# Performance work log

Measured on AMD Instinct MI355X. Metric: run time of the kernel, lower is better.

The kernel has to match this reference:

```python
import jax, jax.numpy as jnp
import numpy as np

N, E = 50000, 1600000
DIM_IN, HEADS, DIM_OUT = 256, 4, 32
NEG_SLOPE = 0.2


def setup_inputs() -> dict:
    key = jax.random.key(0)
    k1, k2, k3, k4, k5, k6 = jax.random.split(key, 6)
    x = jax.random.normal(k1, (N, DIM_IN), dtype=jnp.float32)
    edge_index = jax.random.randint(k2, (2, E), 0, N, dtype=jnp.int64)
    s = 1.0 / np.sqrt(DIM_IN)
    W = jax.random.normal(k3, (DIM_IN, HEADS * DIM_OUT), dtype=jnp.float32) * s
    att_src = jax.random.normal(k4, (HEADS, DIM_OUT), dtype=jnp.float32) * 0.1
    att_dst = jax.random.normal(k5, (HEADS, DIM_OUT), dtype=jnp.float32) * 0.1
    bias = jax.random.normal(k6, (HEADS * DIM_OUT,), dtype=jnp.float32) * 0.01
    return {"x": x, "edge_index": edge_index, "W": W,
            "att_src": att_src, "att_dst": att_dst, "bias": bias}


def reference(x, edge_index, W, att_src, att_dst, bias):
    n = x.shape[0]
    h, c = att_src.shape
    # linear projection, per-head view [N, H, C]
    xp = (x @ W).reshape(n, h, c)
    # per-node attention logits [N, H]
    a_src = jnp.einsum('nhc,hc->nh', xp, att_src)
    a_dst = jnp.einsum('nhc,hc->nh', xp, att_dst)
    # add self loops (PyG default add_self_loops=True)
    loops = jnp.arange(n, dtype=edge_index.dtype)
    src = jnp.concatenate([edge_index[0], loops])  # [E+N]
    dst = jnp.concatenate([edge_index[1], loops])
    # edge attention scores [E+N, H]
    e = jax.nn.leaky_relu(a_src[src] + a_dst[dst], negative_slope=NEG_SLOPE)
    # segment softmax over incoming edges of each dst node
    emax = jax.ops.segment_max(e, dst, num_segments=n)
    ex = jnp.exp(e - emax[dst])
    denom = jax.ops.segment_sum(ex, dst, num_segments=n)
    alpha = ex / denom[dst]  # [E+N, H]
    # weighted scatter-aggregate of src features
    msg = xp[src] * alpha[:, :, None]  # [E+N, H, C]
    out = jax.ops.segment_sum(msg, dst, num_segments=n)  # [N, H, C]
    return out.reshape(n, h * c) + bias
```

## Files before the change

### kernel.cpp

```cpp
#include <hip/hip_runtime.h>
#include <hip/hip_fp16.h>


#define DIN 256
#define HC 128
#define NH 4
#define NEG 0.2f
#define BSH 8
#define BSZ 256

typedef _Float16 half8 __attribute__((ext_vector_type(8)));
typedef _Float16 half2v __attribute__((ext_vector_type(2)));
typedef float f32x4 __attribute__((ext_vector_type(4)));

__global__ void zero_kernel(int* __restrict__ p, int n) {
    int i = blockIdx.x * blockDim.x + threadIdx.x;
    if (i < n) p[i] = 0;
}

__global__ __launch_bounds__(256) void wtrans_kernel(const float* __restrict__ W,
                                                     _Float16* __restrict__ Wt) {
    int i = blockIdx.x * 256 + threadIdx.x;
    int k = i >> 7, c = i & 127;
    Wt[c * 256 + k] = (_Float16)W[i];
}

__global__ __launch_bounds__(256) void proj_kernel(const float* __restrict__ x,
                                                   const _Float16* __restrict__ Wt,
                                                   const float* __restrict__ attS,
                                                   const float* __restrict__ attD,
                                                   __half* __restrict__ xph,
                                                   float* __restrict__ a_src,
                                                   float* __restrict__ a_dst, int n) {
    __shared__ _Float16 smem[8704];
    __shared__ float attSL[128], attDL[128];
    _Float16* xs = smem;
    _Float16* Wl = smem + 2560;
    _Float16* ep = smem;

    const int tid  = threadIdx.x;
    const int node0 = blockIdx.x * 64;
    const int wave = tid >> 6;
    const int lane = tid & 63;
    const int l15  = lane & 15;
    const int quad = lane >> 4;

    if (tid < 128) attSL[tid] = attS[tid];
    else           attDL[tid - 128] = attD[tid - 128];

    f32x4 acc[8];
#pragma unroll
    for (int ct = 0; ct < 8; ++ct) acc[ct] = (f32x4){0.f, 0.f, 0.f, 0.f};

    for (int kt = 0; kt < DIN; kt += 32) {
        __syncthreads();
#pragma unroll
        for (int r = 0; r < 4; ++r) {
            int idx = tid + r * 256;
            int row = idx >> 4;
            int kp  = idx & 15;
            int gn = node0 + row;
            float2 xv = make_float2(0.f, 0.f);
            if (gn < n) xv = *(const float2*)&x[(size_t)gn * DIN + kt + kp * 2];
            half2v p; p[0] = (_Float16)xv.x; p[1] = (_Float16)xv.y;
            *(half2v*)&xs[row * 40 + kp * 2] = p;
        }
#pragma unroll
        for (int r = 0; r < 2; ++r) {
            int id = tid + r * 256;
            int c = id >> 2;
            int q = id & 3;
            half8 wv = *(const half8*)&Wt[(size_t)c * 256 + kt + q * 8];
            *(half8*)&Wl[c * 40 + q * 8] = wv;
        }
        __syncthreads();
        half8 af = *(const half8*)&xs[(wave * 16 + l15) * 40 + quad * 8];
#pragma unroll
        for (int ct = 0; ct < 8; ++ct) {
            half8 bf = *(const half8*)&Wl[(ct * 16 + l15) * 40 + quad * 8];
            acc[ct] = __builtin_amdgcn_mfma_f32_16x16x32_f16(af, bf, acc[ct], 0, 0, 0);
        }
    }
    __syncthreads();
#pragma unroll
    for (int ct = 0; ct < 8; ++ct)
#pragma unroll
        for (int r = 0; r < 4; ++r) {
            int row = wave * 16 + quad * 4 + r;
            ep[row * 136 + ct * 16 + l15] = (_Float16)acc[ct][r];
        }
    __syncthreads();
    {
        int row = tid >> 2, ch = tid & 3;
        int node = node0 + row;
        if (node < n) {
            const uint4* s = (const uint4*)&ep[row * 136 + ch * 32];
            uint4* d = (uint4*)&xph[(size_t)node * HC + ch * 32];
            d[0] = s[0]; d[1] = s[1]; d[2] = s[2]; d[3] = s[3];
        }
    }
    {
        int nl = tid >> 2, h = tid & 3;
        int node = node0 + nl;
        if (node < n) {
            float ps = 0.f, pd = 0.f;
            const _Float16* er = &ep[nl * 136 + h * 32];
#pragma unroll
            for (int c = 0; c < 32; ++c) {
                float v = (float)er[c];
                ps += v * attSL[h * 32 + c];
                pd += v * attDL[h * 32 + c];
            }
            a_src[node * NH + h] = ps;
            a_dst[node * NH + h] = pd;
        }
    }
}

__global__ __launch_bounds__(256) void hist_kernel(const int* __restrict__ ei,
                                                   int* __restrict__ ghist, int e, int n) {
    __shared__ int h[256];
    const int tid = threadIdx.x;
    h[tid] = 0;
    __syncthreads();
    const int base = blockIdx.x * 4096;
#pragma unroll
    for (int j = 0; j < 16; ++j) {
        int i = base + j * 256 + tid;
        if (i < e) {
            int dst = ei[e + i];
            if ((unsigned)dst < (unsigned)n) atomicAdd(&h[dst >> BSH], 1);
        }
    }
    __syncthreads();
    if (h[tid]) atomicAdd(&ghist[tid], h[tid]);
}

__global__ __launch_bounds__(256) void bscan_kernel(const int* __restrict__ ghist,
                                                    int* __restrict__ gbase,
                                                    int* __restrict__ gcur, int nbuck) {
    __shared__ int buf[256];
    const int tid = threadIdx.x;
    int v = (tid < nbuck) ? ghist[tid] : 0;
    buf[tid] = v;
    __syncthreads();
    for (int s = 1; s < 256; s <<= 1) {
        int t = (tid >= s) ? buf[tid - s] : 0;
        __syncthreads();
        buf[tid] += t;
        __syncthreads();
    }
    int excl = buf[tid] - v;
    if (tid < nbuck) { gbase[tid] = excl; gcur[tid] = excl; }
    if (tid == nbuck - 1) gbase[nbuck] = buf[tid];
}

__global__ __launch_bounds__(256) void bin_kernel(const int* __restrict__ ei,
                                                  int* __restrict__ gcur,
                                                  unsigned* __restrict__ binned,
                                                  int e, int n) {
    __shared__ int h[256];
    __shared__ int rbase[256];
    const int tid = threadIdx.x;
    h[tid] = 0;
    __syncthreads();
    const int base = blockIdx.x * 4096;
    unsigned pk[16];
    int bk[16];
#pragma unroll
    for (int j = 0; j < 16; ++j) {
        int i = base + j * 256 + tid;
        bk[j] = -1;
        if (i < e) {
            int src = ei[i];
            int dst = ei[e + i];
            if ((unsigned)dst < (unsigned)n && (unsigned)src < (unsigned)n) {
                bk[j] = dst >> BSH;
                pk[j] = ((unsigned)(dst & (BSZ - 1)) << 24) | (unsigned)src;
                atomicAdd(&h[bk[j]], 1);
            }
        }
    }
    __syncthreads();
    if (h[tid]) rbase[tid] = atomicAdd(&gcur[tid], h[tid]);
    h[tid] = 0;
    __syncthreads();
#pragma unroll
    for (int j = 0; j < 16; ++j) {
        if (bk[j] >= 0) {
            int p = atomicAdd(&h[bk[j]], 1);
            binned[rbase[bk[j]] + p] = pk[j];
        }
    }
}

__global__ __launch_bounds__(256) void csr_kernel(const unsigned* __restrict__ binned,
                                                  const int* __restrict__ gbase,
                                                  int* __restrict__ off,
                                                  unsigned* __restrict__ srt,
                                                  int n, int nbuck) {
    __shared__ int cnt[256], buf[256], cur[256];
    const int tid = threadIdx.x;
    const int b = blockIdx.x;
    const int kb = gbase[b];
    const int ke = gbase[b + 1];
    cnt[tid] = 0;
    __syncthreads();
    for (int i = kb + tid; i < ke; i += 256)
        atomicAdd(&cnt[binned[i] >> 24], 1);
    __syncthreads();
    int v = cnt[tid];
    buf[tid] = v;
    __syncthreads();
    for (int s = 1; s < 256; s <<= 1) {
        int t = (tid >= s) ? buf[tid - s] : 0;
        __syncthreads();
        buf[tid] += t;
        __syncthreads();
    }
    const int excl = kb + buf[tid] - v;
    const int node = b * BSZ + tid;
    if (node < n) off[node] = excl;
    if (tid == 0 && b == nbuck - 1) off[n] = ke;
    cur[tid] = excl;
    __syncthreads();
    const unsigned dbase = (unsigned)(b * BSZ) << 16;
    for (int i = kb + tid; i < ke; i += 256) {
        unsigned pv = binned[i];
        int nl = pv >> 24;
        int pos = atomicAdd(&cur[nl], 1);
        srt[pos] = (dbase + ((unsigned)nl << 16)) | (pv & 0xFFFFu);
    }
}

__global__ __launch_bounds__(256) void escore_kernel(const unsigned* __restrict__ srt,
                                                     const float* __restrict__ a_src,
                                                     const float* __restrict__ a_dst,
                                                     __half* __restrict__ escore,
                                                     int e, int n) {
    int i = blockIdx.x * 256 + threadIdx.x;
    if (i >= e) return;
    unsigned v = srt[i];
    int src = (int)(v & 0xFFFFu);
    int dst = (int)(v >> 16);
    if (src >= n || dst >= n) return;
    const float4 as = *(const float4*)&a_src[(size_t)src * 4];
    const float4 ad = *(const float4*)&a_dst[(size_t)dst * 4];
    float t0 = as.x + ad.x; t0 = (t0 > 0.f) ? t0 : NEG * t0;
    float t1 = as.y + ad.y; t1 = (t1 > 0.f) ? t1 : NEG * t1;
    float t2 = as.z + ad.z; t2 = (t2 > 0.f) ? t2 : NEG * t2;
    float t3 = as.w + ad.w; t3 = (t3 > 0.f) ? t3 : NEG * t3;
    __half2* ep = (__half2*)&escore[(size_t)i * 4];
    ep[0] = __floats2half2_rn(__expf(t0), __expf(t1));
    ep[1] = __floats2half2_rn(__expf(t2), __expf(t3));
}

__global__ __launch_bounds__(256) void agg_kernel(const __half2* __restrict__ xh2,
                                                  const float* __restrict__ a_src,
                                                  const float* __restrict__ a_dst,
                                                  const int* __restrict__ off,
                                                  const unsigned* __restrict__ srt,
                                                  const __half* __restrict__ escore,
                                                  const float* __restrict__ bias,
                                                  float* __restrict__ out, int n) {
    const int gwave = (blockIdx.x * blockDim.x + threadIdx.x) >> 6;
    if (gwave >= n) return;
    const int node = gwave;
    const int lane = threadIdx.x & 63;
    const int h = lane >> 4;

    float e0 = a_src[node * NH + h] + a_dst[node * NH + h];
    e0 = (e0 > 0.f) ? e0 : NEG * e0;
    float g = __expf(e0);
    float2 v = __half22float2(xh2[(size_t)node * 64 + lane]);
    float accx = g * v.x, accy = g * v.y, den = g;

    const int kb = off[node];
    const int ke = off[node + 1];
    int k = kb;
    for (; k + 8 <= ke; k += 8) {
        int s[8];
#pragma unroll
        for (int j = 0; j < 8; ++j) s[j] = (int)(srt[k + j] & 0xFFFFu);
        float sc[8];
#pragma unroll
        for (int j = 0; j < 8; ++j) sc[j] = __half2float(escore[(size_t)(k + j) * 4 + h]);
        __half2 hv[8];
#pragma unroll
        for (int j = 0; j < 8; ++j) hv[j] = xh2[(size_t)s[j] * 64 + lane];
#pragma unroll
        for (int j = 0; j < 8; ++j) {
            float2 vf = __half22float2(hv[j]);
            accx += sc[j] * vf.x;
            accy += sc[j] * vf.y;
            den  += sc[j];
        }
    }
    for (; k < ke; ++k) {
        const int s = (int)(srt[k] & 0xFFFFu);
        const float sc = __half2float(escore[(size_t)k * 4 + h]);
        const float2 vf = __half22float2(xh2[(size_t)s * 64 + lane]);
        accx += sc * vf.x;
        accy += sc * vf.y;
        den  += sc;
    }
    const float2 b2 = ((const float2*)bias)[lane];
    const float inv = 1.0f / den;
    float2 o;
    o.x = accx * inv + b2.x;
    o.y = accy * inv + b2.y;
    ((float2*)out)[(size_t)node * 64 + lane] = o;
}

extern "C" void kernel_launch(void* const* d_in, const int* in_sizes, int n_in,
                              void* d_out, int out_size, void* d_ws, size_t ws_size,
                              hipStream_t stream) {
    if (n_in < 6 || !d_out || !d_ws) return;
    const float* x    = (const float*)d_in[0];
    const int*   ei   = (const int*)d_in[1];
    const float* W    = (const float*)d_in[2];
    const float* attS = (const float*)d_in[3];
    const float* attD = (const float*)d_in[4];
    const float* bias = (const float*)d_in[5];
    float* out = (float*)d_out;

    const int N = in_sizes[0] / DIN;
    const int E = in_sizes[1] / 2;
    if (N <= 0 || E <= 0) return;
    const int NBUCK = (N + BSZ - 1) >> BSH;
    if (NBUCK > 256 || N > 65536) return;

    char* ws = (char*)d_ws;
    size_t off_b = 0;
    auto carve = [&](size_t bytes) {
        size_t p = off_b;
        off_b = (off_b + bytes + 255) & ~(size_t)255;
        return (void*)(ws + p);
    };
    __half*    xph    = (__half*)carve((size_t)N * HC * 2);
    _Float16*  Wt     = (_Float16*)carve((size_t)HC * DIN * 2);
    float*     a_src  = (float*)carve((size_t)N * NH * 4);
    float*     a_dst  = (float*)carve((size_t)N * NH * 4);
    int*       ghist  = (int*)carve(257 * 4);
    int*       gbase  = (int*)carve(257 * 4);
    int*       gcur   = (int*)carve(257 * 4);
    unsigned*  binned = (unsigned*)carve((size_t)E * 4);
    int*       offp   = (int*)carve((size_t)(N + 1) * 4);
    unsigned*  srt    = (unsigned*)carve((size_t)E * 4);
    __half*    escore = (__half*)carve((size_t)E * NH * 2);
    (void)out_size;
    if (off_b > ws_size) return;

    const int ECH = (E + 4095) / 4096;

    zero_kernel<<<2, 256, 0, stream>>>(ghist, 257);
    wtrans_kernel<<<(DIN * HC) / 256, 256, 0, stream>>>(W, Wt);
    proj_kernel<<<(N + 63) / 64, 256, 0, stream>>>(x, Wt, attS, attD, xph, a_src, a_dst, N);
    hist_kernel<<<ECH, 256, 0, stream>>>(ei, ghist, E, N);
    bscan_kernel<<<1, 256, 0, stream>>>(ghist, gbase, gcur, NBUCK);
    bin_kernel<<<ECH, 256, 0, stream>>>(ei, gcur, binned, E, N);
    csr_kernel<<<NBUCK, 256, 0, stream>>>(binned, gbase, offp, srt, N, NBUCK);
    escore_kernel<<<(E + 255) / 256, 256, 0, stream>>>(srt, a_src, a_dst, escore, E, N);
    agg_kernel<<<(N * 64 + 255) / 256, 256, 0, stream>>>((const __half2*)xph, a_src, a_dst,
                                                         offp, srt, escore, bias, out, N);
}
```

Before: 253.8 us.

## Split aggregation wave into four edge groups with 16-byte gathers

The aggregation kernel now splits each node's wave into four 16-lane groups. Each group processes a different edge, gathering 8 halfs per lane with one 16-byte load, and the groups' partial sums are combined with cross-lane shuffles at the end. The CSR kernel moves to 1024-thread blocks so each of its roughly 196 blocks has more threads working through the bucket. The ghist zeroing is folded into the W transpose kernel, which removes one launch. The costs are extra shuffle reductions, more registers for eight accumulators, and divergence in the tail loop when a node's edge count is not a multiple of four.

```diff
diff --git a/kernel.cpp b/kernel.cpp
--- a/kernel.cpp
+++ b/kernel.cpp
@@ -13,14 +13,11 @@
 typedef _Float16 half2v __attribute__((ext_vector_type(2)));
 typedef float f32x4 __attribute__((ext_vector_type(4)));
 
-__global__ void zero_kernel(int* __restrict__ p, int n) {
-    int i = blockIdx.x * blockDim.x + threadIdx.x;
-    if (i < n) p[i] = 0;
-}
-
 __global__ __launch_bounds__(256) void wtrans_kernel(const float* __restrict__ W,
-                                                     _Float16* __restrict__ Wt) {
+                                                     _Float16* __restrict__ Wt,
+                                                     int* __restrict__ ghist) {
     int i = blockIdx.x * 256 + threadIdx.x;
+    if (i < 257) ghist[i] = 0;
     int k = i >> 7, c = i & 127;
     Wt[c * 256 + k] = (_Float16)W[i];
 }
@@ -194,38 +191,40 @@
     }
 }
 
-__global__ __launch_bounds__(256) void csr_kernel(const unsigned* __restrict__ binned,
-                                                  const int* __restrict__ gbase,
-                                                  int* __restrict__ off,
-                                                  unsigned* __restrict__ srt,
-                                                  int n, int nbuck) {
+__global__ __launch_bounds__(1024) void csr_kernel(const unsigned* __restrict__ binned,
+                                                   const int* __restrict__ gbase,
+                                                   int* __restrict__ off,
+                                                   unsigned* __restrict__ srt,
+                                                   int n, int nbuck) {
     __shared__ int cnt[256], buf[256], cur[256];
     const int tid = threadIdx.x;
     const int b = blockIdx.x;
     const int kb = gbase[b];
     const int ke = gbase[b + 1];
-    cnt[tid] = 0;
-    __syncthreads();
-    for (int i = kb + tid; i < ke; i += 256)
+    if (tid < 256) cnt[tid] = 0;
+    __syncthreads();
+    for (int i = kb + tid; i < ke; i += 1024)
         atomicAdd(&cnt[binned[i] >> 24], 1);
     __syncthreads();
-    int v = cnt[tid];
-    buf[tid] = v;
+    int v = 0;
+    if (tid < 256) { v = cnt[tid]; buf[tid] = v; }
     __syncthreads();
     for (int s = 1; s < 256; s <<= 1) {
-        int t = (tid >= s) ? buf[tid - s] : 0;
-        __syncthreads();
-        buf[tid] += t;
-        __syncthreads();
-    }
-    const int excl = kb + buf[tid] - v;
-    const int node = b * BSZ + tid;
-    if (node < n) off[node] = excl;
-    if (tid == 0 && b == nbuck - 1) off[n] = ke;
-    cur[tid] = excl;
+        int t = (tid < 256 && tid >= s) ? buf[tid - s] : 0;
+        __syncthreads();
+        if (tid < 256) buf[tid] += t;
+        __syncthreads();
+    }
+    if (tid < 256) {
+        const int excl = kb + buf[tid] - v;
+        const int node = b * BSZ + tid;
+        if (node < n) off[node] = excl;
+        if (tid == 0 && b == nbuck - 1) off[n] = ke;
+        cur[tid] = excl;
+    }
     __syncthreads();
     const unsigned dbase = (unsigned)(b * BSZ) << 16;
-    for (int i = kb + tid; i < ke; i += 256) {
+    for (int i = kb + tid; i < ke; i += 1024) {
         unsigned pv = binned[i];
         int nl = pv >> 24;
         int pos = atomicAdd(&cur[nl], 1);
@@ -255,7 +254,7 @@
     ep[1] = __floats2half2_rn(__expf(t2), __expf(t3));
 }
 
-__global__ __launch_bounds__(256) void agg_kernel(const __half2* __restrict__ xh2,
+__global__ __launch_bounds__(256) void agg_kernel(const __half* __restrict__ xph,
                                                   const float* __restrict__ a_src,
                                                   const float* __restrict__ a_dst,
                                                   const int* __restrict__ off,
@@ -267,49 +266,81 @@
     if (gwave >= n) return;
     const int node = gwave;
     const int lane = threadIdx.x & 63;
-    const int h = lane >> 4;
-
-    float e0 = a_src[node * NH + h] + a_dst[node * NH + h];
-    e0 = (e0 > 0.f) ? e0 : NEG * e0;
-    float g = __expf(e0);
-    float2 v = __half22float2(xh2[(size_t)node * 64 + lane]);
-    float accx = g * v.x, accy = g * v.y, den = g;
+    const int g = lane >> 4;
+    const int l = lane & 15;
+    const int h = l >> 2;
+
+    float acc[8];
+#pragma unroll
+    for (int c = 0; c < 8; ++c) acc[c] = 0.f;
+    float den = 0.f;
+
+    if (g == 0) {
+        float e0 = a_src[node * NH + h] + a_dst[node * NH + h];
+        e0 = (e0 > 0.f) ? e0 : NEG * e0;
+        float sl = __expf(e0);
+        half8 xv = *(const half8*)&xph[(size_t)node * HC + l * 8];
+#pragma unroll
+        for (int c = 0; c < 8; ++c) acc[c] = sl * (float)xv[c];
+        den = sl;
+    }
 
     const int kb = off[node];
     const int ke = off[node + 1];
-    int k = kb;
-    for (; k + 8 <= ke; k += 8) {
-        int s[8];
-#pragma unroll
-        for (int j = 0; j < 8; ++j) s[j] = (int)(srt[k + j] & 0xFFFFu);
-        float sc[8];
-#pragma unroll
-        for (int j = 0; j < 8; ++j) sc[j] = __half2float(escore[(size_t)(k + j) * 4 + h]);
-        __half2 hv[8];
-#pragma unroll
-        for (int j = 0; j < 8; ++j) hv[j] = xh2[(size_t)s[j] * 64 + lane];
-#pragma unroll
-        for (int j = 0; j < 8; ++j) {
-            float2 vf = __half22float2(hv[j]);
-            accx += sc[j] * vf.x;
-            accy += sc[j] * vf.y;
-            den  += sc[j];
-        }
-    }
-    for (; k < ke; ++k) {
-        const int s = (int)(srt[k] & 0xFFFFu);
-        const float sc = __half2float(escore[(size_t)k * 4 + h]);
-        const float2 vf = __half22float2(xh2[(size_t)s * 64 + lane]);
-        accx += sc * vf.x;
-        accy += sc * vf.y;
-        den  += sc;
-    }
-    const float2 b2 = ((const float2*)bias)[lane];
-    const float inv = 1.0f / den;
-    float2 o;
-    o.x = accx * inv + b2.x;
-    o.y = accy * inv + b2.y;
-    ((float2*)out)[(size_t)node * 64 + lane] = o;
+    int k0 = kb;
+    for (; k0 + 16 <= ke; k0 += 16) {
+        const int kg = k0 + g * 4;
+        unsigned sv[4];
+        float sc[4];
+        half8 hv[4];
+#pragma unroll
+        for (int j = 0; j < 4; ++j) sv[j] = srt[kg + j];
+#pragma unroll
+        for (int j = 0; j < 4; ++j)
+            hv[j] = *(const half8*)&xph[(size_t)(sv[j] & 0xFFFFu) * HC + l * 8];
+#pragma unroll
+        for (int j = 0; j < 4; ++j)
+            sc[j] = __half2float(escore[(size_t)(kg + j) * 4 + h]);
+#pragma unroll
+        for (int j = 0; j < 4; ++j) {
+            const float s = sc[j];
+#pragma unroll
+            for (int c = 0; c < 8; ++c) acc[c] += s * (float)hv[j][c];
+            den += s;
+        }
+    }
+    for (int k = k0 + g; k < ke; k += 4) {
+        const unsigned v = srt[k];
+        const float s = __half2float(escore[(size_t)k * 4 + h]);
+        const half8 hv = *(const half8*)&xph[(size_t)(v & 0xFFFFu) * HC + l * 8];
+#pragma unroll
+        for (int c = 0; c < 8; ++c) acc[c] += s * (float)hv[c];
+        den += s;
+    }
+
+#pragma unroll
+    for (int c = 0; c < 8; ++c) acc[c] += __shfl_xor(acc[c], 16, 64);
+    den += __shfl_xor(den, 16, 64);
+#pragma unroll
+    for (int c = 0; c < 8; ++c) acc[c] += __shfl_xor(acc[c], 32, 64);
+    den += __shfl_xor(den, 32, 64);
+
+    if (lane < 16) {
+        const float inv = 1.0f / den;
+        const float4* b4 = (const float4*)&bias[l * 8];
+        float4 o0, o1;
+        o0.x = acc[0] * inv + b4[0].x;
+        o0.y = acc[1] * inv + b4[0].y;
+        o0.z = acc[2] * inv + b4[0].z;
+        o0.w = acc[3] * inv + b4[0].w;
+        o1.x = acc[4] * inv + b4[1].x;
+        o1.y = acc[5] * inv + b4[1].y;
+        o1.z = acc[6] * inv + b4[1].z;
+        o1.w = acc[7] * inv + b4[1].w;
+        float4* d = (float4*)&out[(size_t)node * HC + l * 8];
+        d[0] = o0;
+        d[1] = o1;
+    }
 }
 
 extern "C" void kernel_launch(void* const* d_in, const int* in_sizes, int n_in,
@@ -353,14 +384,13 @@
 
     const int ECH = (E + 4095) / 4096;
 
-    zero_kernel<<<2, 256, 0, stream>>>(ghist, 257);
-    wtrans_kernel<<<(DIN * HC) / 256, 256, 0, stream>>>(W, Wt);
-    proj_kernel<<<(N + 63) / 64, 256, 0, stream>>>(x, Wt, attS, attD, xph, a_src, a_dst, N);
+    wtrans_kernel<<<(DIN * HC) / 256, 256, 0, stream>>>(W, Wt, ghist);
+    proj_kernel<<<(N + 63) / 64, 256, 0, stream>>>(x, Wt, attS, attD, (__half*)xph, a_src, a_dst, N);
     hist_kernel<<<ECH, 256, 0, stream>>>(ei, ghist, E, N);
     bscan_kernel<<<1, 256, 0, stream>>>(ghist, gbase, gcur, NBUCK);
     bin_kernel<<<ECH, 256, 0, stream>>>(ei, gcur, binned, E, N);
-    csr_kernel<<<NBUCK, 256, 0, stream>>>(binned, gbase, offp, srt, N, NBUCK);
+    csr_kernel<<<NBUCK, 1024, 0, stream>>>(binned, gbase, offp, srt, N, NBUCK);
     escore_kernel<<<(E + 255) / 256, 256, 0, stream>>>(srt, a_src, a_dst, escore, E, N);
-    agg_kernel<<<(N * 64 + 255) / 256, 256, 0, stream>>>((const __half2*)xph, a_src, a_dst,
+    agg_kernel<<<(N * 64 + 255) / 256, 256, 0, stream>>>(xph, a_src, a_dst,
                                                          offp, srt, escore, bias, out, N);
 }
```

Result: faster. 240.6 us (-5.2%).
